# Kernel optimization log

Hardware: AMD Instinct MI355X
Metric: run time of the kernel (lower is better)

The kernel has to match this reference:

```python
import jax, jax.numpy as jnp
import numpy as np

B, L, D, H, DH = 2, 2048, 1024, 16, 64
EPS = 1e-5
ROPE_BASE = 10000.0


def _layernorm(x, w, b):
    mu = jnp.mean(x, axis=-1, keepdims=True)
    var = jnp.var(x, axis=-1, keepdims=True)
    y = (x - mu) * jax.lax.rsqrt(var + EPS)
    y = y * w
    if b is not None:
        y = y + b
    return y


def _rope(x):
    # x: [B, L, H, DH]; GPT-NeoX-style rotation over the full head dim
    inv_freq = 1.0 / (ROPE_BASE ** (jnp.arange(0, DH, 2, dtype=jnp.float32) / DH))  # [DH/2]
    t = jnp.arange(L, dtype=jnp.float32)
    freqs = jnp.outer(t, inv_freq)                       # [L, DH/2]
    cos = jnp.concatenate([jnp.cos(freqs)] * 2, axis=-1)[:, None, :]  # [L, 1, DH]
    sin = jnp.concatenate([jnp.sin(freqs)] * 2, axis=-1)[:, None, :]
    x1, x2 = jnp.split(x, 2, axis=-1)
    rot = jnp.concatenate([-x2, x1], axis=-1)
    return x * cos + rot * sin


def setup_inputs() -> dict:
    key = jax.random.key(0)
    ks = jax.random.split(key, 3)
    x = jax.random.normal(ks[0], (B, L, D), dtype=jnp.float32)
    w_qkv = jax.random.normal(ks[1], (3 * D, D), dtype=jnp.float32) * (D ** -0.5)
    w_out = jax.random.normal(ks[2], (D, D), dtype=jnp.float32) * (D ** -0.5)
    return {
        "x": x,
        "ln_w": jnp.ones((D,), jnp.float32),
        "ln_b": jnp.zeros((D,), jnp.float32),
        "w_qkv": w_qkv,
        "q_ln_w": jnp.ones((D,), jnp.float32),
        "k_ln_w": jnp.ones((D,), jnp.float32),
        "w_out": w_out,
    }


def reference(x, ln_w, ln_b, w_qkv, q_ln_w, k_ln_w, w_out):
    h = _layernorm(x, ln_w, ln_b)                         # [B, L, D]
    qkv = jnp.einsum("bld,ed->ble", h, w_qkv)            # [B, L, 3D]
    q, k, v = jnp.split(qkv, 3, axis=-1)
    q = _layernorm(q, q_ln_w, None)                       # weight-only per-token LN
    k = _layernorm(k, k_ln_w, None)
    q = _rope(q.reshape(B, L, H, DH))                     # [B, L, H, DH]
    k = _rope(k.reshape(B, L, H, DH))
    v = v.reshape(B, L, H, DH)
    ctx = jax.nn.dot_product_attention(q, k, v)           # [B, L, H, DH], scale 1/sqrt(DH)
    ctx = ctx.reshape(B, L, D)
    return jnp.einsum("bld,od->blo", ctx, w_out)
```

## Files before the change

kernel.cpp:

```cpp
#include <hip/hip_runtime.h>
#include <math.h>

#define BB 2
#define LL 2048
#define DD 1024
#define HH 16
#define DHD 64
#define NT (BB*LL)
#define D3 (3*DD)
#define D2 (2*DD)
#define NSPLIT 4
#define KVCH (LL/NSPLIT)

typedef __bf16 bf16x8 __attribute__((ext_vector_type(8)));
typedef float  f32x4  __attribute__((ext_vector_type(4)));

__device__ __forceinline__ f32x4 mfma16(bf16x8 a, bf16x8 b, f32x4 c) {
    return __builtin_amdgcn_mfma_f32_16x16x32_bf16(a, b, c, 0, 0, 0);
}

__device__ __forceinline__ unsigned short f2bf(float f) {
    unsigned int u = __float_as_uint(f);
    u = (u + 0x7FFFu + ((u >> 16) & 1u)) >> 16;
    return (unsigned short)u;
}
__device__ __forceinline__ float bf2f(unsigned short s) {
    return __uint_as_float(((unsigned int)s) << 16);
}

__device__ __forceinline__ void gload16(const void* g, void* l) {
    __builtin_amdgcn_global_load_lds(
        (const __attribute__((address_space(1))) void*)g,
        (__attribute__((address_space(3))) void*)l, 16, 0, 0);
}

__device__ __forceinline__ float wred(float v) {
#pragma unroll
    for (int off = 32; off > 0; off >>= 1) v += __shfl_down(v, off, 64);
    return v;
}

__device__ __forceinline__ unsigned int pack_bf2(float p0, float p1) {
    const unsigned int u0 = __float_as_uint(p0) + 0x8000u;
    const unsigned int u1 = __float_as_uint(p1) + 0x8000u;
    return __builtin_amdgcn_perm(u1, u0, 0x07060302u);
}

__global__ __launch_bounds__(256) void ln_cvt_kernel(
        const float* __restrict__ x, const float* __restrict__ w,
        const float* __restrict__ b, unsigned short* __restrict__ h,
        const float* __restrict__ wq, unsigned short* __restrict__ wqb,
        const float* __restrict__ wo, unsigned short* __restrict__ wob) {
    const int bx = blockIdx.x;
    const int tid = threadIdx.x;
    if (bx >= NT) {
        int i = (bx - NT) * 256 + tid;
        const float* s; unsigned short* d;
        if (i < 786432) { s = wq; d = wqb; }
        else            { i -= 786432; s = wo; d = wob; }
        const float4 v = ((const float4*)s)[i];
        ((ushort4*)d)[i] = make_ushort4(f2bf(v.x), f2bf(v.y), f2bf(v.z), f2bf(v.w));
        return;
    }
    const float4 v = ((const float4*)(x + (size_t)bx * DD))[tid];
    float s = v.x + v.y + v.z + v.w;
    float ss = v.x*v.x + v.y*v.y + v.z*v.z + v.w*v.w;
    s = wred(s); ss = wred(ss);
    __shared__ float red[8];
    if ((tid & 63) == 0) { red[tid >> 6] = s; red[4 + (tid >> 6)] = ss; }
    __syncthreads();
    s  = red[0] + red[1] + red[2] + red[3];
    ss = red[4] + red[5] + red[6] + red[7];
    const float mu  = s * (1.0f / DD);
    const float inv = rsqrtf(ss * (1.0f / DD) - mu * mu + 1e-5f);
    const float4 wv = ((const float4*)w)[tid];
    const float4 bv = ((const float4*)b)[tid];
    *(ushort4*)(h + (size_t)bx * DD + tid * 4) = make_ushort4(
        f2bf((v.x - mu) * inv * wv.x + bv.x),
        f2bf((v.y - mu) * inv * wv.y + bv.y),
        f2bf((v.z - mu) * inv * wv.z + bv.z),
        f2bf((v.w - mu) * inv * wv.w + bv.w));
}

__global__ __launch_bounds__(256) void gemm_qkv(
        const unsigned short* __restrict__ A, const unsigned short* __restrict__ B,
        unsigned short* __restrict__ qk, unsigned short* __restrict__ vt) {
    const int K = DD;
    __shared__ unsigned short As[128 * 32];
    __shared__ unsigned short Bs[128 * 32];
    const int tid = threadIdx.x;
    const int w = tid >> 6, lane = tid & 63;
    const int l15 = lane & 15, quad = lane >> 4;
    const int wr = w >> 1, wc = w & 1;
    const int m0 = blockIdx.y << 7, n0 = blockIdx.x << 7;

    const int srow = w * 32 + (lane >> 2);
    const int skel = (lane & 3) << 3;
    const unsigned short* gA = A + (size_t)(m0 + srow) * K + skel;
    const unsigned short* gB = B + (size_t)(n0 + srow) * K + skel;
    unsigned short* lA = &As[w * 1024];
    unsigned short* lB = &Bs[w * 1024];

    f32x4 acc[4][4];
#pragma unroll
    for (int i = 0; i < 4; i++)
#pragma unroll
        for (int j = 0; j < 4; j++) acc[i][j] = (f32x4){0.f, 0.f, 0.f, 0.f};

    for (int k0 = 0; k0 < K; k0 += 32) {
        gload16(gA + k0,                 lA);
        gload16(gA + k0 + (size_t)16*K,  lA + 512);
        gload16(gB + k0,                 lB);
        gload16(gB + k0 + (size_t)16*K,  lB + 512);
        __syncthreads();
        bf16x8 af[4], bg[4];
#pragma unroll
        for (int i = 0; i < 4; i++) {
            af[i] = *(const bf16x8*)&As[(wr*64 + i*16 + l15) * 32 + quad*8];
            bg[i] = *(const bf16x8*)&Bs[(wc*64 + i*16 + l15) * 32 + quad*8];
        }
#pragma unroll
        for (int i = 0; i < 4; i++)
#pragma unroll
            for (int j = 0; j < 4; j++)
                acc[i][j] = mfma16(af[i], bg[j], acc[i][j]);
        __syncthreads();
    }
    if (n0 < D2) {
#pragma unroll
        for (int i = 0; i < 4; i++) {
            const int mrow = m0 + wr*64 + i*16 + quad*4;
#pragma unroll
            for (int j = 0; j < 4; j++) {
                const int ncol = n0 + wc*64 + j*16 + l15;
#pragma unroll
                for (int r = 0; r < 4; r++)
                    qk[(size_t)(mrow + r) * D2 + ncol] = f2bf(acc[i][j][r]);
            }
        }
    } else {
#pragma unroll
        for (int i = 0; i < 4; i++) {
            const int mrow = m0 + wr*64 + i*16 + quad*4;
            const int bb = mrow >> 11, l = mrow & (LL - 1);
#pragma unroll
            for (int j = 0; j < 4; j++) {
                const int nv = n0 + wc*64 + j*16 + l15 - D2;
                const int hh = nv >> 6, dh = nv & 63;
                *(ushort4*)&vt[((size_t)(bb*HH + hh) * DHD + dh) * LL + l] =
                    make_ushort4(f2bf(acc[i][j][0]), f2bf(acc[i][j][1]),
                                 f2bf(acc[i][j][2]), f2bf(acc[i][j][3]));
            }
        }
    }
}

__global__ __launch_bounds__(256) void gemm_out(
        const unsigned short* __restrict__ A, const unsigned short* __restrict__ B,
        float* __restrict__ C, int M, int N, int K) {
    __shared__ unsigned short As[64 * 32];
    __shared__ unsigned short Bs[128 * 32];
    const int tid = threadIdx.x;
    const int w = tid >> 6, lane = tid & 63;
    const int l15 = lane & 15, quad = lane >> 4;
    const int wr = w >> 1, wc = w & 1;
    const int m0 = blockIdx.y << 6, n0 = blockIdx.x << 7;
    const int skel = (lane & 3) << 3;
    const unsigned short* gA = A + (size_t)(m0 + w*16 + (lane >> 2)) * K + skel;
    const unsigned short* gB = B + (size_t)(n0 + w*32 + (lane >> 2)) * K + skel;
    unsigned short* lA = &As[w * 512];
    unsigned short* lB = &Bs[w * 1024];
    f32x4 acc[2][4];
#pragma unroll
    for (int i = 0; i < 2; i++)
#pragma unroll
        for (int j = 0; j < 4; j++) acc[i][j] = (f32x4){0.f, 0.f, 0.f, 0.f};
    for (int k0 = 0; k0 < K; k0 += 32) {
        gload16(gA + k0,                 lA);
        gload16(gB + k0,                 lB);
        gload16(gB + k0 + (size_t)16*K,  lB + 512);
        __syncthreads();
        bf16x8 af[2], bg[4];
#pragma unroll
        for (int i = 0; i < 2; i++)
            af[i] = *(const bf16x8*)&As[(wr*32 + i*16 + l15) * 32 + quad*8];
#pragma unroll
        for (int j = 0; j < 4; j++)
            bg[j] = *(const bf16x8*)&Bs[(wc*64 + j*16 + l15) * 32 + quad*8];
#pragma unroll
        for (int i = 0; i < 2; i++)
#pragma unroll
            for (int j = 0; j < 4; j++)
                acc[i][j] = mfma16(af[i], bg[j], acc[i][j]);
        __syncthreads();
    }
#pragma unroll
    for (int i = 0; i < 2; i++) {
        const int mrow = m0 + wr*32 + i*16 + quad*4;
#pragma unroll
        for (int j = 0; j < 4; j++) {
            const int ncol = n0 + wc*64 + j*16 + l15;
#pragma unroll
            for (int r = 0; r < 4; r++)
                C[(size_t)(mrow + r) * N + ncol] = acc[i][j][r];
        }
    }
}

__global__ __launch_bounds__(256) void qk_rope_kernel(
        const unsigned short* __restrict__ qk,
        const float* __restrict__ qw, const float* __restrict__ kw,
        unsigned short* __restrict__ qarr, unsigned short* __restrict__ karr) {
    const int t = blockIdx.x;
    const int l = t & (LL - 1), b = t >> 11;
    const int tid = threadIdx.x;
    const unsigned short* base = qk + (size_t)t * D2;
    const ushort4 qu = *(const ushort4*)(base + tid * 4);
    const ushort4 ku = *(const ushort4*)(base + DD + tid * 4);
    const float q[4] = {bf2f(qu.x), bf2f(qu.y), bf2f(qu.z), bf2f(qu.w)};
    const float k[4] = {bf2f(ku.x), bf2f(ku.y), bf2f(ku.z), bf2f(ku.w)};
    float sq = q[0]+q[1]+q[2]+q[3], ssq = q[0]*q[0]+q[1]*q[1]+q[2]*q[2]+q[3]*q[3];
    float sk = k[0]+k[1]+k[2]+k[3], ssk = k[0]*k[0]+k[1]*k[1]+k[2]*k[2]+k[3]*k[3];
    sq = wred(sq); ssq = wred(ssq); sk = wred(sk); ssk = wred(ssk);
    __shared__ float red[16];
    __shared__ float qs[DD], ks[DD];
    const int wid = tid >> 6;
    if ((tid & 63) == 0) { red[wid] = sq; red[4+wid] = ssq; red[8+wid] = sk; red[12+wid] = ssk; }
    __syncthreads();
    sq = red[0]+red[1]+red[2]+red[3];    ssq = red[4]+red[5]+red[6]+red[7];
    sk = red[8]+red[9]+red[10]+red[11];  ssk = red[12]+red[13]+red[14]+red[15];
    const float muq = sq * (1.f/DD), invq = rsqrtf(ssq*(1.f/DD) - muq*muq + 1e-5f);
    const float muk = sk * (1.f/DD), invk = rsqrtf(ssk*(1.f/DD) - muk*muk + 1e-5f);
    const float4 qwv = ((const float4*)qw)[tid];
    const float4 kwv = ((const float4*)kw)[tid];
    const float qwa[4] = {qwv.x, qwv.y, qwv.z, qwv.w};
    const float kwa[4] = {kwv.x, kwv.y, kwv.z, kwv.w};
    float qn[4], kn[4];
#pragma unroll
    for (int e = 0; e < 4; e++) {
        qn[e] = (q[e] - muq) * invq * qwa[e];
        kn[e] = (k[e] - muk) * invk * kwa[e];
    }
    *(float4*)&qs[tid*4] = make_float4(qn[0], qn[1], qn[2], qn[3]);
    *(float4*)&ks[tid*4] = make_float4(kn[0], kn[1], kn[2], kn[3]);
    __syncthreads();
    const int d = tid * 4, j0 = d & 63;
    const bool first = (j0 < 32);
    const int pt = first ? (tid + 8) : (tid - 8);
    const float4 qp4 = *(const float4*)&qs[pt*4];
    const float4 kp4 = *(const float4*)&ks[pt*4];
    const float qb[4] = {qp4.x, qp4.y, qp4.z, qp4.w};
    const float kb[4] = {kp4.x, kp4.y, kp4.z, kp4.w};
    const float lf = (float)l;
    const float QS = 0.125f * 1.44269504088896340736f;
    unsigned short oq[4], ok[4];
#pragma unroll
    for (int e = 0; e < 4; e++) {
        const float fi   = (float)((j0 & 31) + e);
        const float freq = expf(fi * (-0.28782313662425576f));
        const float ang  = lf * freq;
        const float c = cosf(ang), sn = sinf(ang);
        float vq, vk;
        if (first) { vq = qn[e]*c - qb[e]*sn; vk = kn[e]*c - kb[e]*sn; }
        else       { vq = qn[e]*c + qb[e]*sn; vk = kn[e]*c + kb[e]*sn; }
        oq[e] = f2bf(vq * QS);
        ok[e] = f2bf(vk);
    }
    const int hh = tid >> 4;
    const int dh = (tid * 4) & 63;
    const size_t ro = ((size_t)(b*HH + hh) * LL + l) * DHD + dh;
    *(ushort4*)(qarr + ro) = make_ushort4(oq[0], oq[1], oq[2], oq[3]);
    *(ushort4*)(karr + ro) = make_ushort4(ok[0], ok[1], ok[2], ok[3]);
}

__global__ __launch_bounds__(256, 4) void attn_kernel(
        const unsigned short* __restrict__ qarr,
        const unsigned short* __restrict__ karr,
        const unsigned short* __restrict__ vt,
        unsigned short* __restrict__ op0, unsigned short* __restrict__ op1,
        unsigned short* __restrict__ op2, unsigned short* __restrict__ op3,
        float* __restrict__ lpart) {
    const int x = blockIdx.x;
    const int g  = (x & 7) | ((x >> 7) << 3);
    const int qblk = (x >> 3) & 15;
    const int s = g & 3, bh = g >> 2;
    const int b = bh >> 4, h = bh & 15;
    const int q0 = qblk << 7;
    const int kvbase = s * KVCH;
    const int tid = threadIdx.x, w = tid >> 6, lane = tid & 63;
    const int l15 = lane & 15, quad = lane >> 4;

    __shared__ unsigned short Ks[64 * 64];
    __shared__ unsigned short Vs[64 * 64];
    __shared__ unsigned short Pw[4][16][72];

    const unsigned short* kbase = karr + ((size_t)bh * LL + kvbase) * DHD;
    const unsigned short* vbase = vt   + (size_t)bh * DHD * LL + kvbase;

    bf16x8 qf[2][2];
    {
        const unsigned short* qp = qarr + ((size_t)bh*LL + q0 + w*32 + l15) * DHD + quad*8;
#pragma unroll
        for (int qt = 0; qt < 2; qt++)
#pragma unroll
            for (int c = 0; c < 2; c++)
                qf[qt][c] = *(const bf16x8*)(qp + qt*16*DHD + c*32);
    }

    bf16x8 ones;
#pragma unroll
    for (int i = 0; i < 8; i++) ones[i] = (__bf16)1.0f;

    const int r8 = lane >> 3, sc = lane & 7;
    f32x4 o[2][4], lacc[2];
#pragma unroll
    for (int qt = 0; qt < 2; qt++) {
        lacc[qt] = (f32x4){0.f, 0.f, 0.f, 0.f};
#pragma unroll
        for (int nt = 0; nt < 4; nt++) o[qt][nt] = (f32x4){0.f, 0.f, 0.f, 0.f};
    }

#pragma unroll
    for (int rd = 0; rd < 2; rd++) {
        const int row = w*8 + rd*32 + r8;
        const int chunk = sc ^ (row & 7);
        gload16(kbase + (size_t)row * DHD + chunk*8, (char*)Ks + w*1024 + rd*4096);
        gload16(vbase + (size_t)row * LL + chunk*8,  (char*)Vs + w*1024 + rd*4096);
    }

    for (int kt = 0; kt < KVCH/64; kt++) {
        __syncthreads();
        bf16x8 kf[4][2], vf[4][2];
#pragma unroll
        for (int t = 0; t < 4; t++)
#pragma unroll
            for (int c = 0; c < 2; c++) {
                const int slot = (quad + c*4) ^ (l15 & 7);
                kf[t][c] = *(const bf16x8*)&Ks[(t*16 + l15) * DHD + slot*8];
                vf[t][c] = *(const bf16x8*)&Vs[(t*16 + l15) * DHD + slot*8];
            }
        __syncthreads();
        if (kt + 1 < KVCH/64) {
#pragma unroll
            for (int rd = 0; rd < 2; rd++) {
                const int row = w*8 + rd*32 + r8;
                const int chunk = sc ^ (row & 7);
                gload16(kbase + ((size_t)((kt+1)*64 + row)) * DHD + chunk*8,
                        (char*)Ks + w*1024 + rd*4096);
                gload16(vbase + (size_t)row * LL + (kt+1)*64 + chunk*8,
                        (char*)Vs + w*1024 + rd*4096);
            }
        }

#pragma unroll
        for (int qt = 0; qt < 2; qt++) {
            f32x4 st[4];
#pragma unroll
            for (int t = 0; t < 4; t++) {
                f32x4 z = (f32x4){-64.f, -64.f, -64.f, -64.f};
                z = mfma16(kf[t][0], qf[qt][0], z);
                z = mfma16(kf[t][1], qf[qt][1], z);
                st[t] = z;
            }
#pragma unroll
            for (int t = 0; t < 4; t++) {
                const float p0 = __builtin_amdgcn_exp2f(st[t][0]);
                const float p1 = __builtin_amdgcn_exp2f(st[t][1]);
                const float p2 = __builtin_amdgcn_exp2f(st[t][2]);
                const float p3 = __builtin_amdgcn_exp2f(st[t][3]);
                uint2 pk;
                pk.x = pack_bf2(p0, p1);
                pk.y = pack_bf2(p2, p3);
                *(uint2*)&Pw[w][l15][t*16 + quad*4] = pk;
            }
            const bf16x8 ap0 = *(const bf16x8*)&Pw[w][l15][quad*8];
            const bf16x8 ap1 = *(const bf16x8*)&Pw[w][l15][32 + quad*8];
            lacc[qt] = mfma16(ap0, ones, lacc[qt]);
            lacc[qt] = mfma16(ap1, ones, lacc[qt]);
#pragma unroll
            for (int nt = 0; nt < 4; nt++) {
                f32x4 t0 = o[qt][nt];
                t0 = mfma16(ap0, vf[nt][0], t0);
                t0 = mfma16(ap1, vf[nt][1], t0);
                o[qt][nt] = t0;
            }
        }
    }

    unsigned short* op = (s == 0) ? op0 : (s == 1) ? op1 : (s == 2) ? op2 : op3;
#pragma unroll
    for (int qt = 0; qt < 2; qt++) {
#pragma unroll
        for (int r = 0; r < 4; r++) {
            const int qrow = q0 + w*32 + qt*16 + quad*4 + r;
            const size_t token = (size_t)b * LL + qrow;
#pragma unroll
            for (int nt = 0; nt < 4; nt++)
                op[token * DD + h*DHD + nt*16 + l15] = f2bf(o[qt][nt][r]);
        }
        if (l15 == 0) {
#pragma unroll
            for (int r = 0; r < 4; r++)
                lpart[((size_t)s * BB*HH + bh) * LL + q0 + w*32 + qt*16 + quad*4 + r] =
                    lacc[qt][r];
        }
    }
}

__global__ __launch_bounds__(256) void combine_kernel(
        const unsigned short* __restrict__ op0, const unsigned short* __restrict__ op1,
        const unsigned short* __restrict__ op2, const unsigned short* __restrict__ op3,
        const float* __restrict__ lpart, unsigned short* __restrict__ ctx) {
    const int token = blockIdx.x;
    const int tid = threadIdx.x;
    const int b = token >> 11, l = token & (LL - 1);
    const int h = tid >> 4;
    const size_t idx = (size_t)token * DD + tid * 4;
    const ushort4 a0 = *(const ushort4*)(op0 + idx);
    const ushort4 a1 = *(const ushort4*)(op1 + idx);
    const ushort4 a2 = *(const ushort4*)(op2 + idx);
    const ushort4 a3 = *(const ushort4*)(op3 + idx);
    const size_t lbase = (size_t)(b*HH + h) * LL + l;
    const float lsum = lpart[lbase] + lpart[(size_t)BB*HH*LL + lbase]
                     + lpart[2*(size_t)BB*HH*LL + lbase] + lpart[3*(size_t)BB*HH*LL + lbase];
    const float inv = 1.0f / lsum;
    *(ushort4*)(ctx + idx) = make_ushort4(
        f2bf((bf2f(a0.x) + bf2f(a1.x) + bf2f(a2.x) + bf2f(a3.x)) * inv),
        f2bf((bf2f(a0.y) + bf2f(a1.y) + bf2f(a2.y) + bf2f(a3.y)) * inv),
        f2bf((bf2f(a0.z) + bf2f(a1.z) + bf2f(a2.z) + bf2f(a3.z)) * inv),
        f2bf((bf2f(a0.w) + bf2f(a1.w) + bf2f(a2.w) + bf2f(a3.w)) * inv));
}

extern "C" void kernel_launch(void* const* d_in, const int* in_sizes, int n_in,
                              void* d_out, int out_size, void* d_ws, size_t ws_size,
                              hipStream_t stream) {
    const float* x      = (const float*)d_in[0];
    const float* ln_w   = (const float*)d_in[1];
    const float* ln_b   = (const float*)d_in[2];
    const float* w_qkv  = (const float*)d_in[3];
    const float* q_ln_w = (const float*)d_in[4];
    const float* k_ln_w = (const float*)d_in[5];
    const float* w_out  = (const float*)d_in[6];
    float* out = (float*)d_out;

    char* ws = (char*)d_ws;
    unsigned short* hb    = (unsigned short*)ws;
    unsigned short* karr  = (unsigned short*)ws;
    unsigned short* qk    = (unsigned short*)(ws + ((size_t)8  << 20));
    unsigned short* op0   = (unsigned short*)(ws + ((size_t)8  << 20));
    unsigned short* op1   = (unsigned short*)(ws + ((size_t)16 << 20));
    unsigned short* vtp   = (unsigned short*)(ws + ((size_t)24 << 20));
    unsigned short* qarr  = (unsigned short*)(ws + ((size_t)32 << 20));
    unsigned short* ctxb  = (unsigned short*)(ws + ((size_t)32 << 20));
    unsigned short* op2   = (unsigned short*)(ws + ((size_t)40 << 20));
    unsigned short* op3   = (unsigned short*)(ws + ((size_t)48 << 20));
    unsigned short* wqb   = (unsigned short*)(ws + ((size_t)56 << 20));
    float*          lpart = (float*)(ws + ((size_t)56 << 20));
    unsigned short* wob   = (unsigned short*)(ws + ((size_t)62 << 20));

    ln_cvt_kernel<<<NT + 4096, 256, 0, stream>>>(x, ln_w, ln_b, hb,
                                                 w_qkv, wqb, w_out, wob);
    gemm_qkv<<<dim3(D3/128, NT/128), 256, 0, stream>>>(hb, wqb, qk, vtp);
    qk_rope_kernel<<<NT, 256, 0, stream>>>(qk, q_ln_w, k_ln_w, qarr, karr);
    attn_kernel<<<2048, 256, 0, stream>>>(qarr, karr, vtp, op0, op1, op2, op3, lpart);
    combine_kernel<<<NT, 256, 0, stream>>>(op0, op1, op2, op3, lpart, ctxb);
    gemm_out<<<dim3(DD/128, NT/64), 256, 0, stream>>>(ctxb, wob, out, NT, DD, DD);
}
```

Before: 278.8 us.

## Fuse split-KV combine into attention via intra-block two-way KV split

The attention kernel now handles a 64-query tile per block. Two wave pairs each process half of the KV sequence (1024 keys) with 32-key stages, and their partial outputs and row sums are reduced through shared memory in a union-aliased buffer. The normalised bf16 context is written directly with coalesced stores, which removes the separate combine kernel and the four global partial-output buffers with their write and read traffic. RoPE also switches to hardware exp2, sin and cos on range-reduced revolutions in place of expf, sinf and cosf. The cost is fewer blocks (1024 vs 2048), smaller per-stage tiles, extra barriers, and some loss of precision in the angle computation.

```diff
diff --git a/kernel.cpp b/kernel.cpp
--- a/kernel.cpp
+++ b/kernel.cpp
@@ -9,8 +9,6 @@
 #define NT (BB*LL)
 #define D3 (3*DD)
 #define D2 (2*DD)
-#define NSPLIT 4
-#define KVCH (LL/NSPLIT)
 
 typedef __bf16 bf16x8 __attribute__((ext_vector_type(8)));
 typedef float  f32x4  __attribute__((ext_vector_type(4)));
@@ -257,9 +255,12 @@
 #pragma unroll
     for (int e = 0; e < 4; e++) {
         const float fi   = (float)((j0 & 31) + e);
-        const float freq = expf(fi * (-0.28782313662425576f));
-        const float ang  = lf * freq;
-        const float c = cosf(ang), sn = sinf(ang);
+        const float frev = __builtin_amdgcn_exp2f(fi * -0.41524101186092029f)
+                         * 0.15915494309189535f;
+        float rev = lf * frev;
+        rev -= floorf(rev);
+        const float sn = __builtin_amdgcn_sinf(rev);
+        const float c  = __builtin_amdgcn_cosf(rev);
         float vq, vk;
         if (first) { vq = qn[e]*c - qb[e]*sn; vk = kn[e]*c - kb[e]*sn; }
         else       { vq = qn[e]*c + qb[e]*sn; vk = kn[e]*c + kb[e]*sn; }
@@ -277,29 +278,36 @@
         const unsigned short* __restrict__ qarr,
         const unsigned short* __restrict__ karr,
         const unsigned short* __restrict__ vt,
-        unsigned short* __restrict__ op0, unsigned short* __restrict__ op1,
-        unsigned short* __restrict__ op2, unsigned short* __restrict__ op3,
-        float* __restrict__ lpart) {
+        unsigned short* __restrict__ ctxb) {
     const int x = blockIdx.x;
-    const int g  = (x & 7) | ((x >> 7) << 3);
-    const int qblk = (x >> 3) & 15;
-    const int s = g & 3, bh = g >> 2;
-    const int b = bh >> 4, h = bh & 15;
-    const int q0 = qblk << 7;
-    const int kvbase = s * KVCH;
+    const int bh = (x & 7) | ((x >> 8) << 3);
+    const int qblk = (x >> 3) & 31;
+    const int b = bh >> 4, hh = bh & 15;
+    const int q0 = qblk << 6;
     const int tid = threadIdx.x, w = tid >> 6, lane = tid & 63;
     const int l15 = lane & 15, quad = lane >> 4;
-
-    __shared__ unsigned short Ks[64 * 64];
-    __shared__ unsigned short Vs[64 * 64];
-    __shared__ unsigned short Pw[4][16][72];
-
-    const unsigned short* kbase = karr + ((size_t)bh * LL + kvbase) * DHD;
-    const unsigned short* vbase = vt   + (size_t)bh * DHD * LL + kvbase;
+    const int h  = w >> 1;
+    const int wr = w & 1;
+
+    __shared__ union {
+        struct {
+            unsigned short Ks[2 * 32 * 64];
+            unsigned short Vs[2 * 64 * 32];
+            unsigned short Pw[4][16][40];
+        } m;
+        struct {
+            float red[64][64];
+            float lred[64];
+            unsigned short red_bf[64][72];
+        } e;
+    } sm;
+
+    const unsigned short* kbase = karr + ((size_t)bh * LL + h * 1024) * DHD;
+    const unsigned short* vbase = vt   + (size_t)bh * DHD * LL + h * 1024;
 
     bf16x8 qf[2][2];
     {
-        const unsigned short* qp = qarr + ((size_t)bh*LL + q0 + w*32 + l15) * DHD + quad*8;
+        const unsigned short* qp = qarr + ((size_t)bh*LL + q0 + wr*32 + l15) * DHD + quad*8;
 #pragma unroll
         for (int qt = 0; qt < 2; qt++)
 #pragma unroll
@@ -311,7 +319,7 @@
 #pragma unroll
     for (int i = 0; i < 8; i++) ones[i] = (__bf16)1.0f;
 
-    const int r8 = lane >> 3, sc = lane & 7;
+    const int p = w & 1;
     f32x4 o[2][4], lacc[2];
 #pragma unroll
     for (int qt = 0; qt < 2; qt++) {
@@ -320,50 +328,57 @@
         for (int nt = 0; nt < 4; nt++) o[qt][nt] = (f32x4){0.f, 0.f, 0.f, 0.f};
     }
 
-#pragma unroll
-    for (int rd = 0; rd < 2; rd++) {
-        const int row = w*8 + rd*32 + r8;
-        const int chunk = sc ^ (row & 7);
-        gload16(kbase + (size_t)row * DHD + chunk*8, (char*)Ks + w*1024 + rd*4096);
-        gload16(vbase + (size_t)row * LL + chunk*8,  (char*)Vs + w*1024 + rd*4096);
-    }
-
-    for (int kt = 0; kt < KVCH/64; kt++) {
-        __syncthreads();
-        bf16x8 kf[4][2], vf[4][2];
-#pragma unroll
-        for (int t = 0; t < 4; t++)
+    const int kr8 = lane >> 3, kc = lane & 7;
+    const int vr4 = lane >> 2, vc = lane & 3;
+#define STAGE(KT)                                                                   \
+    {                                                                               \
+        const int kt_ = (KT);                                                       \
+        _Pragma("unroll")                                                           \
+        for (int rd = 0; rd < 2; rd++) {                                            \
+            const int row = p*16 + rd*8 + kr8;                                      \
+            gload16(kbase + (size_t)(kt_*32 + row) * DHD + (kc ^ kr8) * 8,          \
+                    &sm.m.Ks[h*2048 + (p*16 + rd*8) * 64]);                         \
+        }                                                                           \
+        _Pragma("unroll")                                                           \
+        for (int rv = 0; rv < 2; rv++) {                                            \
+            const int dhrow = p*32 + rv*16 + vr4;                                   \
+            gload16(vbase + (size_t)dhrow * LL + kt_*32 + (vc ^ (vr4 & 3)) * 8,     \
+                    &sm.m.Vs[h*2048 + (p*32 + rv*16) * 32]);                        \
+        }                                                                           \
+    }
+
+    STAGE(0);
+
+    for (int kt = 0; kt < 32; kt++) {
+        __syncthreads();
+        bf16x8 kf[2][2], vf[4];
+#pragma unroll
+        for (int t = 0; t < 2; t++)
 #pragma unroll
             for (int c = 0; c < 2; c++) {
                 const int slot = (quad + c*4) ^ (l15 & 7);
-                kf[t][c] = *(const bf16x8*)&Ks[(t*16 + l15) * DHD + slot*8];
-                vf[t][c] = *(const bf16x8*)&Vs[(t*16 + l15) * DHD + slot*8];
+                kf[t][c] = *(const bf16x8*)&sm.m.Ks[h*2048 + (t*16 + l15) * 64 + slot*8];
             }
-        __syncthreads();
-        if (kt + 1 < KVCH/64) {
-#pragma unroll
-            for (int rd = 0; rd < 2; rd++) {
-                const int row = w*8 + rd*32 + r8;
-                const int chunk = sc ^ (row & 7);
-                gload16(kbase + ((size_t)((kt+1)*64 + row)) * DHD + chunk*8,
-                        (char*)Ks + w*1024 + rd*4096);
-                gload16(vbase + (size_t)row * LL + (kt+1)*64 + chunk*8,
-                        (char*)Vs + w*1024 + rd*4096);
-            }
-        }
+#pragma unroll
+        for (int nt = 0; nt < 4; nt++) {
+            const int slot = quad ^ (l15 & 3);
+            vf[nt] = *(const bf16x8*)&sm.m.Vs[h*2048 + (nt*16 + l15) * 32 + slot*8];
+        }
+        __syncthreads();
+        if (kt + 1 < 32) STAGE(kt + 1);
 
 #pragma unroll
         for (int qt = 0; qt < 2; qt++) {
-            f32x4 st[4];
-#pragma unroll
-            for (int t = 0; t < 4; t++) {
+            f32x4 st[2];
+#pragma unroll
+            for (int t = 0; t < 2; t++) {
                 f32x4 z = (f32x4){-64.f, -64.f, -64.f, -64.f};
                 z = mfma16(kf[t][0], qf[qt][0], z);
                 z = mfma16(kf[t][1], qf[qt][1], z);
                 st[t] = z;
             }
 #pragma unroll
-            for (int t = 0; t < 4; t++) {
+            for (int t = 0; t < 2; t++) {
                 const float p0 = __builtin_amdgcn_exp2f(st[t][0]);
                 const float p1 = __builtin_amdgcn_exp2f(st[t][1]);
                 const float p2 = __builtin_amdgcn_exp2f(st[t][2]);
@@ -371,64 +386,58 @@
                 uint2 pk;
                 pk.x = pack_bf2(p0, p1);
                 pk.y = pack_bf2(p2, p3);
-                *(uint2*)&Pw[w][l15][t*16 + quad*4] = pk;
+                *(uint2*)&sm.m.Pw[w][l15][t*16 + quad*4] = pk;
             }
-            const bf16x8 ap0 = *(const bf16x8*)&Pw[w][l15][quad*8];
-            const bf16x8 ap1 = *(const bf16x8*)&Pw[w][l15][32 + quad*8];
-            lacc[qt] = mfma16(ap0, ones, lacc[qt]);
-            lacc[qt] = mfma16(ap1, ones, lacc[qt]);
-#pragma unroll
-            for (int nt = 0; nt < 4; nt++) {
-                f32x4 t0 = o[qt][nt];
-                t0 = mfma16(ap0, vf[nt][0], t0);
-                t0 = mfma16(ap1, vf[nt][1], t0);
-                o[qt][nt] = t0;
-            }
-        }
-    }
-
-    unsigned short* op = (s == 0) ? op0 : (s == 1) ? op1 : (s == 2) ? op2 : op3;
-#pragma unroll
-    for (int qt = 0; qt < 2; qt++) {
-#pragma unroll
-        for (int r = 0; r < 4; r++) {
-            const int qrow = q0 + w*32 + qt*16 + quad*4 + r;
-            const size_t token = (size_t)b * LL + qrow;
+            const bf16x8 ap = *(const bf16x8*)&sm.m.Pw[w][l15][quad*8];
+            lacc[qt] = mfma16(ap, ones, lacc[qt]);
 #pragma unroll
             for (int nt = 0; nt < 4; nt++)
-                op[token * DD + h*DHD + nt*16 + l15] = f2bf(o[qt][nt][r]);
-        }
-        if (l15 == 0) {
+                o[qt][nt] = mfma16(ap, vf[nt], o[qt][nt]);
+        }
+    }
+#undef STAGE
+
+    __syncthreads();
+    if (h == 1) {
+#pragma unroll
+        for (int qt = 0; qt < 2; qt++) {
+#pragma unroll
+            for (int nt = 0; nt < 4; nt++)
+#pragma unroll
+                for (int r = 0; r < 4; r++)
+                    sm.e.red[wr*32 + qt*16 + quad*4 + r][nt*16 + l15] = o[qt][nt][r];
+            if (l15 == 0)
+#pragma unroll
+                for (int r = 0; r < 4; r++)
+                    sm.e.lred[wr*32 + qt*16 + quad*4 + r] = lacc[qt][r];
+        }
+    }
+    __syncthreads();
+    if (h == 0) {
+#pragma unroll
+        for (int qt = 0; qt < 2; qt++) {
+            float inv[4];
 #pragma unroll
             for (int r = 0; r < 4; r++)
-                lpart[((size_t)s * BB*HH + bh) * LL + q0 + w*32 + qt*16 + quad*4 + r] =
-                    lacc[qt][r];
-        }
-    }
-}
-
-__global__ __launch_bounds__(256) void combine_kernel(
-        const unsigned short* __restrict__ op0, const unsigned short* __restrict__ op1,
-        const unsigned short* __restrict__ op2, const unsigned short* __restrict__ op3,
-        const float* __restrict__ lpart, unsigned short* __restrict__ ctx) {
-    const int token = blockIdx.x;
-    const int tid = threadIdx.x;
-    const int b = token >> 11, l = token & (LL - 1);
-    const int h = tid >> 4;
-    const size_t idx = (size_t)token * DD + tid * 4;
-    const ushort4 a0 = *(const ushort4*)(op0 + idx);
-    const ushort4 a1 = *(const ushort4*)(op1 + idx);
-    const ushort4 a2 = *(const ushort4*)(op2 + idx);
-    const ushort4 a3 = *(const ushort4*)(op3 + idx);
-    const size_t lbase = (size_t)(b*HH + h) * LL + l;
-    const float lsum = lpart[lbase] + lpart[(size_t)BB*HH*LL + lbase]
-                     + lpart[2*(size_t)BB*HH*LL + lbase] + lpart[3*(size_t)BB*HH*LL + lbase];
-    const float inv = 1.0f / lsum;
-    *(ushort4*)(ctx + idx) = make_ushort4(
-        f2bf((bf2f(a0.x) + bf2f(a1.x) + bf2f(a2.x) + bf2f(a3.x)) * inv),
-        f2bf((bf2f(a0.y) + bf2f(a1.y) + bf2f(a2.y) + bf2f(a3.y)) * inv),
-        f2bf((bf2f(a0.z) + bf2f(a1.z) + bf2f(a2.z) + bf2f(a3.z)) * inv),
-        f2bf((bf2f(a0.w) + bf2f(a1.w) + bf2f(a2.w) + bf2f(a3.w)) * inv));
+                inv[r] = 1.0f / (lacc[qt][r] + sm.e.lred[wr*32 + qt*16 + quad*4 + r]);
+#pragma unroll
+            for (int nt = 0; nt < 4; nt++)
+#pragma unroll
+                for (int r = 0; r < 4; r++) {
+                    const int tok = wr*32 + qt*16 + quad*4 + r;
+                    const float v = (o[qt][nt][r] + sm.e.red[tok][nt*16 + l15]) * inv[r];
+                    sm.e.red_bf[tok][nt*16 + l15] = f2bf(v);
+                }
+        }
+    }
+    __syncthreads();
+#pragma unroll
+    for (int i = 0; i < 2; i++) {
+        const int idx = tid + 256*i;
+        const int token = idx >> 3, ch = idx & 7;
+        const uint4 vdat = *(const uint4*)&sm.e.red_bf[token][ch*8];
+        *(uint4*)&ctxb[(size_t)(b*LL + q0 + token) * DD + hh*DHD + ch*8] = vdat;
+    }
 }
 
 extern "C" void kernel_launch(void* const* d_in, const int* in_sizes, int n_in,
@@ -447,22 +456,16 @@
     unsigned short* hb    = (unsigned short*)ws;
     unsigned short* karr  = (unsigned short*)ws;
     unsigned short* qk    = (unsigned short*)(ws + ((size_t)8  << 20));
-    unsigned short* op0   = (unsigned short*)(ws + ((size_t)8  << 20));
-    unsigned short* op1   = (unsigned short*)(ws + ((size_t)16 << 20));
+    unsigned short* ctxb  = (unsigned short*)(ws + ((size_t)8  << 20));
     unsigned short* vtp   = (unsigned short*)(ws + ((size_t)24 << 20));
     unsigned short* qarr  = (unsigned short*)(ws + ((size_t)32 << 20));
-    unsigned short* ctxb  = (unsigned short*)(ws + ((size_t)32 << 20));
-    unsigned short* op2   = (unsigned short*)(ws + ((size_t)40 << 20));
-    unsigned short* op3   = (unsigned short*)(ws + ((size_t)48 << 20));
-    unsigned short* wqb   = (unsigned short*)(ws + ((size_t)56 << 20));
-    float*          lpart = (float*)(ws + ((size_t)56 << 20));
-    unsigned short* wob   = (unsigned short*)(ws + ((size_t)62 << 20));
+    unsigned short* wqb   = (unsigned short*)(ws + ((size_t)40 << 20));
+    unsigned short* wob   = (unsigned short*)(ws + ((size_t)46 << 20));
 
     ln_cvt_kernel<<<NT + 4096, 256, 0, stream>>>(x, ln_w, ln_b, hb,
                                                  w_qkv, wqb, w_out, wob);
     gemm_qkv<<<dim3(D3/128, NT/128), 256, 0, stream>>>(hb, wqb, qk, vtp);
     qk_rope_kernel<<<NT, 256, 0, stream>>>(qk, q_ln_w, k_ln_w, qarr, karr);
-    attn_kernel<<<2048, 256, 0, stream>>>(qarr, karr, vtp, op0, op1, op2, op3, lpart);
-    combine_kernel<<<NT, 256, 0, stream>>>(op0, op1, op2, op3, lpart, ctxb);
+    attn_kernel<<<1024, 256, 0, stream>>>(qarr, karr, vtp, ctxb);
     gemm_out<<<dim3(DD/128, NT/64), 256, 0, stream>>>(ctxb, wob, out, NT, DD, DD);
 }
```

Measured after the change: 249.1 us. 1.12x faster.
